# Performance work log

Hardware: AMD Instinct MI355X
Metric: run time of the kernel (lower is better)

Reference implementation:

```python
import jax, jax.numpy as jnp
import numpy as np
from itertools import combinations

NUM_FIELDS = 32
EMB = 64
# static pair index lists for combinations(range(NUM_FIELDS), 2)
_PAIRS = np.array(list(combinations(range(NUM_FIELDS), 2)), dtype=np.int32)  # (496, 2)
I_IDX = jnp.asarray(_PAIRS[:, 0])
J_IDX = jnp.asarray(_PAIRS[:, 1])


def bilinear_each(feats, W):
    # feats: (B, F, E); W: (F-1, E, E) with torch Linear convention y = x @ W[i].T
    # transform fields 0..F-2 with their own weight
    t = jnp.einsum('bfe,foe->bfo', feats[:, :NUM_FIELDS - 1, :], W)  # (B, F-1, E)
    # pair (i, j): t[:, i] * feats[:, j]
    return t[:, I_IDX, :] * feats[:, J_IDX, :]  # (B, P, E)


def se_block(x, se_w1, se_w2):
    # x: (B, F, E)
    Z = jnp.mean(x, axis=-1)                      # (B, F)
    A = jax.nn.relu(Z @ se_w1.T)                  # (B, F//r)
    A = jax.nn.sigmoid(A @ se_w2.T)               # (B, F)
    return x * A[:, :, None]


def setup_inputs() -> dict:
    key = jax.random.key(0)
    ks = jax.random.split(key, 12)
    B, F, E = 1024, NUM_FIELDS, EMB
    P = F * (F - 1) // 2
    d_in = 2 * P * E  # 63488
    h1, h2, nc = 1024, 512, 1
    red = max(1, F // 8)
    s = lambda *sh: 1.0 / np.sqrt(sh[-1])
    inp = {
        'x': jax.random.normal(ks[0], (B, F, E), dtype=jnp.float32),
        'W_bil1': jax.random.normal(ks[1], (F - 1, E, E), jnp.float32) * s(E),
        'W_bil2': jax.random.normal(ks[2], (F - 1, E, E), jnp.float32) * s(E),
        'se_w1': jax.random.normal(ks[3], (red, F), jnp.float32) * s(F),
        'se_w2': jax.random.normal(ks[4], (F, red), jnp.float32) * s(red),
        'fc0_w': jax.random.normal(ks[5], (h1, d_in), jnp.float32) * s(d_in),
        'fc0_b': jnp.zeros((h1,), jnp.float32),
        'fc1_w': jax.random.normal(ks[6], (h2, h1), jnp.float32) * s(h1),
        'fc1_b': jnp.zeros((h2,), jnp.float32),
        'fc2_w': jax.random.normal(ks[7], (nc, h2), jnp.float32) * s(h2),
        'fc2_b': jnp.zeros((nc,), jnp.float32),
    }
    return inp


def reference(x, W_bil1, W_bil2, se_w1, se_w2, fc0_w, fc0_b, fc1_w, fc1_b, fc2_w, fc2_b):
    f1 = bilinear_each(x, W_bil1)                    # (B, P, E)
    f2 = bilinear_each(se_block(x, se_w1, se_w2), W_bil2)  # (B, P, E)
    feat = jnp.concatenate([f1, f2], axis=1).reshape(x.shape[0], -1)  # (B, 2*P*E)
    h = jax.nn.relu(feat @ fc0_w.T + fc0_b)
    h = jax.nn.relu(h @ fc1_w.T + fc1_b)
    y = jax.nn.sigmoid(h @ fc2_w.T + fc2_b)
    return y
```

## Files before the change

kernel.cpp:

```cpp
#include <hip/hip_runtime.h>
#include <hip/hip_bf16.h>
#include <stdint.h>


typedef __attribute__((ext_vector_type(4))) int   int4v;
typedef __attribute__((ext_vector_type(4))) unsigned uint4v;
typedef __attribute__((ext_vector_type(4))) float f32x4;

__device__ __forceinline__ unsigned short f32_bf16(float f) {
  unsigned u = __builtin_bit_cast(unsigned, f);
  u = (u + 0x7fffu + ((u >> 16) & 1u)) >> 16;
  return (unsigned short)u;
}
__device__ __forceinline__ unsigned pk_bf16(float lo, float hi) {
  return (unsigned)f32_bf16(lo) | ((unsigned)f32_bf16(hi) << 16);
}

__global__ __launch_bounds__(256) void se_kernel(
    const float* __restrict__ x, const float* __restrict__ w1,
    const float* __restrict__ w2, float* __restrict__ scale) {
  __shared__ float Z[32];
  __shared__ float A1[4];
  int b = blockIdx.x;
  int t = threadIdx.x;
  int f = t >> 3, sub = t & 7;
  const float4* xp = (const float4*)(x + (size_t)b * 2048 + f * 64 + sub * 8);
  float4 v0 = xp[0], v1 = xp[1];
  float s = v0.x + v0.y + v0.z + v0.w + v1.x + v1.y + v1.z + v1.w;
  s += __shfl_down(s, 4, 8);
  s += __shfl_down(s, 2, 8);
  s += __shfl_down(s, 1, 8);
  if (sub == 0) Z[f] = s * (1.0f / 64.0f);
  __syncthreads();
  if (t < 4) {
    float a = 0.f;
#pragma unroll
    for (int ff = 0; ff < 32; ++ff) a += Z[ff] * w1[t * 32 + ff];
    A1[t] = fmaxf(a, 0.f);
  }
  __syncthreads();
  if (t < 32) {
    float a = 0.f;
#pragma unroll
    for (int r = 0; r < 4; ++r) a += A1[r] * w2[t * 4 + r];
    scale[b * 32 + t] = 1.f / (1.f + expf(-a));
  }
}

__global__ __launch_bounds__(256) void t_kernel(
    const float* __restrict__ x, const float* __restrict__ W1,
    const float* __restrict__ W2, const float* __restrict__ scale,
    float* __restrict__ t1, float* __restrict__ t2) {
  __shared__ float Wl[64 * 65];
  __shared__ float xs[64 * 65];
  int f = blockIdx.x;
  int b0 = blockIdx.y * 64;
  int which = blockIdx.z;
  const float* W = (which ? W2 : W1) + (size_t)f * 4096;
  float* tout = which ? t2 : t1;
  int t = threadIdx.x;
#pragma unroll
  for (int it = 0; it < 16; ++it) {
    int idx = it * 256 + t;
    int o = idx >> 6, e = idx & 63;
    Wl[o * 65 + e] = W[idx];
  }
#pragma unroll
  for (int it = 0; it < 16; ++it) {
    int idx = it * 256 + t;
    int bl = idx >> 6, e = idx & 63;
    float v = x[(size_t)(b0 + bl) * 2048 + f * 64 + e];
    if (which) v *= scale[(b0 + bl) * 32 + f];
    xs[bl * 65 + e] = v;
  }
  __syncthreads();
  int o = t & 63, g = t >> 6;
  float sum[16];
#pragma unroll
  for (int r = 0; r < 16; ++r) sum[r] = 0.f;
#pragma unroll 4
  for (int e = 0; e < 64; ++e) {
    float wv = Wl[o * 65 + e];
#pragma unroll
    for (int r = 0; r < 16; ++r) sum[r] += xs[(g * 16 + r) * 65 + e] * wv;
  }
#pragma unroll
  for (int r = 0; r < 16; ++r)
    tout[(size_t)(b0 + g * 16 + r) * 1984 + f * 64 + o] = sum[r];
}

__global__ __launch_bounds__(256) void feat_kernel(
    const float* __restrict__ x, const float* __restrict__ t1,
    const float* __restrict__ t2, const float* __restrict__ scale,
    unsigned short* __restrict__ feat) {
  int gid = blockIdx.x * 256 + threadIdx.x;
  int b = gid / 7936;
  int rem = gid - b * 7936;
  int s = rem >> 3;
  int e0 = (rem & 7) * 8;
  int which = (s >= 496) ? 1 : 0;
  int p = s - (which ? 496 : 0);
  int i = (int)((63.0f - sqrtf((float)(3969 - 8 * p))) * 0.5f);
  while ((i * (63 - i)) / 2 > p) --i;
  while (((i + 1) * (62 - i)) / 2 <= p) ++i;
  int j = i + 1 + (p - (i * (63 - i)) / 2);
  const float* tp = (which ? t2 : t1) + (size_t)b * 1984 + i * 64 + e0;
  const float* xp = x + (size_t)b * 2048 + j * 64 + e0;
  float sc = which ? scale[b * 32 + j] : 1.0f;
  float4 ta = *(const float4*)tp, tb = *(const float4*)(tp + 4);
  float4 xa = *(const float4*)xp, xb = *(const float4*)(xp + 4);
  uint4v o;
  o.x = pk_bf16(ta.x * xa.x * sc, ta.y * xa.y * sc);
  o.y = pk_bf16(ta.z * xa.z * sc, ta.w * xa.w * sc);
  o.z = pk_bf16(tb.x * xb.x * sc, tb.y * xb.y * sc);
  o.w = pk_bf16(tb.z * xb.z * sc, tb.w * xb.w * sc);
  *(uint4v*)(feat + (size_t)b * 63488 + s * 64 + e0) = o;
}

#define BM 256
#define BN 128
#define BK 64

__device__ __forceinline__ void mfma_bf16(f32x4& d, int4v a, int4v b) {
  asm volatile("v_mfma_f32_16x16x32_bf16 %0, %1, %2, %0"
               : "+v"(d) : "v"(a), "v"(b));
}

__global__ __launch_bounds__(256, 2) void gemm_bt(
    const unsigned short* __restrict__ A, const float* __restrict__ B,
    float* __restrict__ Cp, int M, int N, int K, int kz) {
  __shared__ unsigned short sA[BM * BK];
  __shared__ unsigned short sB[BN * BK];
  int tid = threadIdx.x;
  int lane = tid & 63, wave = tid >> 6;
  int n0 = blockIdx.x * BN, m0 = blockIdx.y * BM;
  int z = blockIdx.z;
  int wr = (wave >> 1) * 128, wc = (wave & 1) * 64;
  int l15 = lane & 15, l4 = lane >> 4;
  f32x4 acc[8][4];
#pragma unroll
  for (int i = 0; i < 8; ++i)
#pragma unroll
    for (int j = 0; j < 4; ++j) acc[i][j] = (f32x4){0.f, 0.f, 0.f, 0.f};

  int kend = z * kz + kz;
  for (int kt = z * kz; kt < kend; kt += BK) {
#pragma unroll
    for (int it = 0; it < 8; ++it) {
      int c = it * 256 + tid;
      int r = c >> 3, p = c & 7;
      int gcol = (p ^ (r & 7)) * 8;
      const unsigned short* gp = A + (size_t)(m0 + r) * K + kt + gcol;
      __builtin_amdgcn_global_load_lds(
          (const __attribute__((address_space(1))) void*)gp,
          (__attribute__((address_space(3))) void*)(&sA[c * 8]), 16, 0, 0);
    }
#pragma unroll
    for (int it = 0; it < 4; ++it) {
      int c = it * 256 + tid;
      int r = c >> 3, l = c & 7;
      const float* gp = B + (size_t)(n0 + r) * K + kt + l * 8;
      float4 f0 = *(const float4*)gp;
      float4 f1 = *(const float4*)(gp + 4);
      uint4v q;
      q.x = pk_bf16(f0.x, f0.y); q.y = pk_bf16(f0.z, f0.w);
      q.z = pk_bf16(f1.x, f1.y); q.w = pk_bf16(f1.z, f1.w);
      int p = l ^ (r & 7);
      *(uint4v*)(&sB[(r * 8 + p) * 8]) = q;
    }
    __syncthreads();
#pragma unroll
    for (int kk = 0; kk < 2; ++kk) {
      int lc = kk * 4 + l4;
      int4v av[8], bv[4];
#pragma unroll
      for (int i = 0; i < 8; ++i) {
        int ar = wr + i * 16 + l15;
        av[i] = *(const int4v*)&sA[(ar * 8 + (lc ^ (ar & 7))) * 8];
      }
#pragma unroll
      for (int j = 0; j < 4; ++j) {
        int br = wc + j * 16 + l15;
        bv[j] = *(const int4v*)&sB[(br * 8 + (lc ^ (br & 7))) * 8];
      }
#pragma unroll
      for (int i = 0; i < 8; ++i)
#pragma unroll
        for (int j = 0; j < 4; ++j) mfma_bf16(acc[i][j], av[i], bv[j]);
    }
    __syncthreads();
  }
  asm volatile("s_nop 7\n\ts_nop 7\n\ts_nop 7" ::: "memory");
  float* cp = Cp + (size_t)z * M * N;
#pragma unroll
  for (int i = 0; i < 8; ++i) {
    int rbase = m0 + wr + i * 16 + l4 * 4;
#pragma unroll
    for (int j = 0; j < 4; ++j) {
      int cc = n0 + wc + j * 16 + l15;
#pragma unroll
      for (int r = 0; r < 4; ++r)
        cp[(size_t)(rbase + r) * N + cc] = acc[i][j][r];
    }
  }
}

__global__ __launch_bounds__(256) void reduce_bias_act(
    const float* __restrict__ parts, const float* __restrict__ bias,
    int MN, int nmask, int nz, unsigned short* __restrict__ out_bf,
    float* __restrict__ out_f) {
  int idx = blockIdx.x * 256 + threadIdx.x;
  if (idx >= MN) return;
  float s = 0.f;
  for (int z = 0; z < nz; ++z) s += parts[(size_t)z * MN + idx];
  s += bias[idx & nmask];
  s = fmaxf(s, 0.f);
  if (out_bf) out_bf[idx] = f32_bf16(s);
  else out_f[idx] = s;
}

__global__ __launch_bounds__(256) void fc2_kernel(
    const float* __restrict__ h2, const float* __restrict__ w,
    const float* __restrict__ b, float* __restrict__ out) {
  int wave = threadIdx.x >> 6, lane = threadIdx.x & 63;
  int row = blockIdx.x * 4 + wave;
  const float4* hp = (const float4*)(h2 + (size_t)row * 512);
  const float4* wp = (const float4*)w;
  int i0 = lane * 2;
  float4 a0 = hp[i0], a1 = hp[i0 + 1];
  float4 w0 = wp[i0], w1 = wp[i0 + 1];
  float s = a0.x * w0.x + a0.y * w0.y + a0.z * w0.z + a0.w * w0.w +
            a1.x * w1.x + a1.y * w1.y + a1.z * w1.z + a1.w * w1.w;
#pragma unroll
  for (int off = 32; off > 0; off >>= 1) s += __shfl_down(s, off);
  if (lane == 0) out[row] = 1.f / (1.f + expf(-(s + b[0])));
}

extern "C" void kernel_launch(void* const* d_in, const int* in_sizes, int n_in,
                              void* d_out, int out_size, void* d_ws, size_t ws_size,
                              hipStream_t stream) {
  const float* x     = (const float*)d_in[0];
  const float* Wb1   = (const float*)d_in[1];
  const float* Wb2   = (const float*)d_in[2];
  const float* se_w1 = (const float*)d_in[3];
  const float* se_w2 = (const float*)d_in[4];
  const float* fc0_w = (const float*)d_in[5];
  const float* fc0_b = (const float*)d_in[6];
  const float* fc1_w = (const float*)d_in[7];
  const float* fc1_b = (const float*)d_in[8];
  const float* fc2_w = (const float*)d_in[9];
  const float* fc2_b = (const float*)d_in[10];
  (void)in_sizes; (void)n_in; (void)out_size; (void)ws_size;

  char* ws = (char*)d_ws;
  float*          scale = (float*)(ws + 0);
  float*          t1    = (float*)(ws + 131072);
  float*          t2    = (float*)(ws + 8257536);
  unsigned short* feat  = (unsigned short*)(ws + 16384000);
  float*          hp    = (float*)(ws + 146407424);
  unsigned short* h1b   = (unsigned short*)(ws + 213516288);
  float*          h2    = (float*)(ws + 215613440);
  float*          out   = (float*)d_out;

  se_kernel<<<1024, 256, 0, stream>>>(x, se_w1, se_w2, scale);
  t_kernel<<<dim3(31, 16, 2), 256, 0, stream>>>(x, Wb1, Wb2, scale, t1, t2);
  feat_kernel<<<31744, 256, 0, stream>>>(x, t1, t2, scale, feat);
  gemm_bt<<<dim3(8, 4, 16), 256, 0, stream>>>(feat, fc0_w, hp, 1024, 1024, 63488, 3968);
  reduce_bias_act<<<4096, 256, 0, stream>>>(hp, fc0_b, 1024 * 1024, 1023, 16, h1b, nullptr);
  gemm_bt<<<dim3(4, 4, 16), 256, 0, stream>>>(h1b, fc1_w, hp, 1024, 512, 1024, 64);
  reduce_bias_act<<<2048, 256, 0, stream>>>(hp, fc1_b, 1024 * 512, 511, 16, nullptr, h2);
  fc2_kernel<<<256, 256, 0, stream>>>(h2, fc2_w, fc2_b, out);
}
```

Measured before the change: 583.4 us.

## Add dedicated double-buffered fc0 GEMM with direct-to-LDS loads and 8-way split-K

```diff
diff --git a/kernel.cpp b/kernel.cpp
--- a/kernel.cpp
+++ b/kernel.cpp
@@ -14,6 +14,11 @@
 }
 __device__ __forceinline__ unsigned pk_bf16(float lo, float hi) {
   return (unsigned)f32_bf16(lo) | ((unsigned)f32_bf16(hi) << 16);
+}
+__device__ __forceinline__ unsigned cvt_pk(float lo, float hi) {
+  unsigned r;
+  asm("v_cvt_pk_bf16_f32 %0, %1, %2" : "=v"(r) : "v"(lo), "v"(hi));
+  return r;
 }
 
 __global__ __launch_bounds__(256) void se_kernel(
@@ -117,14 +122,144 @@
   *(uint4v*)(feat + (size_t)b * 63488 + s * 64 + e0) = o;
 }
 
+__device__ __forceinline__ void mfma_bf16(f32x4& d, int4v a, int4v b) {
+  asm volatile("v_mfma_f32_16x16x32_bf16 %0, %1, %2, %0"
+               : "+v"(d) : "v"(a), "v"(b));
+}
+
+#define FBM 256
+#define FBN 128
+#define FBK 64
+
+__device__ __forceinline__ void fc0_phase(
+    const unsigned short* __restrict__ sAb, const float* __restrict__ sBb,
+    int kk, int wr, int wc, int l15, int l4, f32x4 (&acc)[8][2]) {
+  int4v av[8];
+#pragma unroll
+  for (int i = 0; i < 8; ++i) {
+    int ar = wr + i * 16 + l15;
+    int slot = (kk * 4 + l4) ^ (ar & 7);
+    av[i] = *(const int4v*)&sAb[(ar * 8 + slot) * 8];
+  }
+  int4v bv[2];
+#pragma unroll
+  for (int j = 0; j < 2; ++j) {
+    int br = wc + j * 16 + l15;
+    int ps = (kk * 4 + l4) ^ (br & 7);
+    const float4* fp = (const float4*)&sBb[br * 64 + ps * 8];
+    float4 f0 = fp[0], f1 = fp[1];
+    uint4v q;
+    q.x = cvt_pk(f0.x, f0.y);
+    q.y = cvt_pk(f0.z, f0.w);
+    q.z = cvt_pk(f1.x, f1.y);
+    q.w = cvt_pk(f1.z, f1.w);
+    bv[j] = __builtin_bit_cast(int4v, q);
+  }
+  __builtin_amdgcn_s_setprio(1);
+#pragma unroll
+  for (int i = 0; i < 8; ++i)
+#pragma unroll
+    for (int j = 0; j < 2; ++j) mfma_bf16(acc[i][j], av[i], bv[j]);
+  __builtin_amdgcn_s_setprio(0);
+}
+
+__global__ __launch_bounds__(512, 2) void gemm_fc0(
+    const unsigned short* __restrict__ A, const float* __restrict__ B,
+    float* __restrict__ Cp, int M, int N, int K, int kz) {
+  __shared__ unsigned short sA[2][FBM * FBK];
+  __shared__ float          sB[2][FBN * FBK];
+  int tid = threadIdx.x;
+  int lane = tid & 63, wave = tid >> 6;
+  int bid = blockIdx.x;
+  int z = bid & 7;
+  int mn = bid >> 3;
+  int m0 = (mn & 3) * FBM;
+  int n0 = (mn >> 2) * FBN;
+  int wm = wave >> 2, wn = wave & 3;
+  int wr = wm * 128, wc = wn * 32;
+  int l15 = lane & 15, l4 = lane >> 4;
+  int kbase = z * kz;
+  int nt = kz / FBK;
+
+  f32x4 acc[8][2];
+#pragma unroll
+  for (int i = 0; i < 8; ++i)
+#pragma unroll
+    for (int j = 0; j < 2; ++j) acc[i][j] = (f32x4){0.f, 0.f, 0.f, 0.f};
+
+  size_t aOff[4]; int aDst[4];
+  size_t bOff[4]; int bDst[4];
+#pragma unroll
+  for (int it = 0; it < 4; ++it) {
+    int c = it * 512 + tid;
+    {
+      int r = c >> 3, p = c & 7;
+      aOff[it] = (size_t)(m0 + r) * K + ((p ^ (r & 7)) << 3);
+      aDst[it] = c * 8;
+    }
+    {
+      int r = c >> 4, s = c & 15;
+      bOff[it] = (size_t)(n0 + r) * K + ((s ^ ((r & 7) << 1)) << 2);
+      bDst[it] = c * 4;
+    }
+  }
+
+#define FC0_STAGE_HALF(buf, kt, h)                                             \
+  _Pragma("unroll") for (int it = (h) * 2; it < (h) * 2 + 2; ++it) {           \
+    __builtin_amdgcn_global_load_lds(                                          \
+        (const __attribute__((address_space(1))) void*)(A + aOff[it] + (kt)),  \
+        (__attribute__((address_space(3))) void*)(&sA[buf][aDst[it]]), 16, 0, 0); \
+    __builtin_amdgcn_global_load_lds(                                          \
+        (const __attribute__((address_space(1))) void*)(B + bOff[it] + (kt)),  \
+        (__attribute__((address_space(3))) void*)(&sB[buf][bDst[it]]), 16, 0, 0); \
+  }
+
+  FC0_STAGE_HALF(0, kbase, 0)
+  FC0_STAGE_HALF(0, kbase, 1)
+
+  for (int t = 0; t < nt; ++t) {
+    int cur = t & 1, nxt = cur ^ 1;
+    int ktn = kbase + (t + 1) * FBK;
+    bool pf = (t + 1 < nt);
+    if (pf) {
+      FC0_STAGE_HALF(nxt, ktn, 0)
+      asm volatile("s_waitcnt vmcnt(4)" ::: "memory");
+    } else {
+      asm volatile("s_waitcnt vmcnt(0)" ::: "memory");
+    }
+    __builtin_amdgcn_sched_barrier(0);
+    __builtin_amdgcn_s_barrier();
+    __builtin_amdgcn_sched_barrier(0);
+    fc0_phase(sA[cur], sB[cur], 0, wr, wc, l15, l4, acc);
+    __builtin_amdgcn_sched_barrier(0);
+    __builtin_amdgcn_s_barrier();
+    __builtin_amdgcn_sched_barrier(0);
+    if (pf) { FC0_STAGE_HALF(nxt, ktn, 1) }
+    fc0_phase(sA[cur], sB[cur], 1, wr, wc, l15, l4, acc);
+    __builtin_amdgcn_sched_barrier(0);
+    __builtin_amdgcn_s_barrier();
+    __builtin_amdgcn_sched_barrier(0);
+  }
+#undef FC0_STAGE_HALF
+
+  asm volatile("s_nop 7\n\ts_nop 7\n\ts_nop 7" ::: "memory");
+  float* cp = Cp + (size_t)z * M * N;
+#pragma unroll
+  for (int i = 0; i < 8; ++i) {
+    int rbase = m0 + wr + i * 16 + l4 * 4;
+#pragma unroll
+    for (int j = 0; j < 2; ++j) {
+      int cc = n0 + wc + j * 16 + l15;
+#pragma unroll
+      for (int r = 0; r < 4; ++r)
+        cp[(size_t)(rbase + r) * N + cc] = acc[i][j][r];
+    }
+  }
+}
+
 #define BM 256
 #define BN 128
 #define BK 64
-
-__device__ __forceinline__ void mfma_bf16(f32x4& d, int4v a, int4v b) {
-  asm volatile("v_mfma_f32_16x16x32_bf16 %0, %1, %2, %0"
-               : "+v"(d) : "v"(a), "v"(b));
-}
 
 __global__ __launch_bounds__(256, 2) void gemm_bt(
     const unsigned short* __restrict__ A, const float* __restrict__ B,
@@ -265,8 +400,8 @@
   se_kernel<<<1024, 256, 0, stream>>>(x, se_w1, se_w2, scale);
   t_kernel<<<dim3(31, 16, 2), 256, 0, stream>>>(x, Wb1, Wb2, scale, t1, t2);
   feat_kernel<<<31744, 256, 0, stream>>>(x, t1, t2, scale, feat);
-  gemm_bt<<<dim3(8, 4, 16), 256, 0, stream>>>(feat, fc0_w, hp, 1024, 1024, 63488, 3968);
-  reduce_bias_act<<<4096, 256, 0, stream>>>(hp, fc0_b, 1024 * 1024, 1023, 16, h1b, nullptr);
+  gemm_fc0<<<256, 512, 0, stream>>>(feat, fc0_w, hp, 1024, 1024, 63488, 7936);
+  reduce_bias_act<<<4096, 256, 0, stream>>>(hp, fc0_b, 1024 * 1024, 1023, 8, h1b, nullptr);
   gemm_bt<<<dim3(4, 4, 16), 256, 0, stream>>>(h1b, fc1_w, hp, 1024, 512, 1024, 64);
   reduce_bias_act<<<2048, 256, 0, stream>>>(hp, fc1_b, 1024 * 512, 511, 16, nullptr, h2);
   fc2_kernel<<<256, 256, 0, stream>>>(h2, fc2_w, fc2_b, out);
```

After: 701.3 us. 1.2x slower.
